# Kernel tuning notes

Measured on AMD Instinct MI355X. Metric: run time of the kernel, lower is better.

## Reference

```python
import jax, jax.numpy as jnp
import numpy as np

N_NODES = 100000
N_EDGES = 1600000
D = 64


def setup_inputs() -> dict:
    key = jax.random.key(0)
    ks = jax.random.split(key, 9)
    x = jax.random.normal(ks[0], (N_NODES, D), dtype=jnp.float32)
    edge_index = jax.random.randint(ks[1], (2, N_EDGES), 0, N_NODES, dtype=jnp.int64)
    edge_attr = jax.random.uniform(ks[2], (N_EDGES,), dtype=jnp.float32)

    def glorot(k, din, dout):
        s = np.sqrt(6.0 / (din + dout)).astype(np.float32)
        return jax.random.uniform(k, (din, dout), jnp.float32, -s, s)

    return {
        "x": x,
        "edge_index": edge_index,
        "edge_attr": edge_attr,
        "W1": glorot(ks[3], D, D), "b1": jnp.zeros((D,), jnp.float32),
        "W2": glorot(ks[4], D, D), "b2": jnp.zeros((D,), jnp.float32),
        "W3": glorot(ks[5], D, D), "b3": jnp.zeros((D,), jnp.float32),
    }


def _gcn_norm(edge_index, edge_weight, n):
    # PyG gcn_norm: add self-loops (weight 1), symmetric D^-1/2 A D^-1/2 normalization.
    src = jnp.concatenate([edge_index[0], jnp.arange(n, dtype=edge_index.dtype)])
    dst = jnp.concatenate([edge_index[1], jnp.arange(n, dtype=edge_index.dtype)])
    w = jnp.concatenate([edge_weight, jnp.ones((n,), edge_weight.dtype)])
    deg = jax.ops.segment_sum(w, dst, num_segments=n)  # in-degree with self-loops
    dinv = jnp.where(deg > 0, jax.lax.rsqrt(deg), 0.0)
    norm = dinv[src] * w * dinv[dst]  # [E+N]
    return src, dst, norm


def _gcn_conv(x, W, b, src, dst, norm, n):
    h = x @ W                                   # linear transform first (PyG GCNConv)
    msg = h[src] * norm[:, None]                # gather + per-edge scale
    out = jax.ops.segment_sum(msg, dst, num_segments=n)  # scatter-add aggregate
    return out + b


def reference(x, edge_index, edge_attr, W1, b1, W2, b2, W3, b3):
    n = x.shape[0]
    src, dst, norm = _gcn_norm(edge_index, edge_attr, n)
    h = jax.nn.relu(_gcn_conv(x, W1, b1, src, dst, norm, n))
    h = jax.nn.relu(_gcn_conv(h, W2, b2, src, dst, norm, n))
    return _gcn_conv(h, W3, b3, src, dst, norm, n)
```

## Files before the change

kernel.cpp:

```cpp
#include <hip/hip_runtime.h>

#define NN 100000
#define NE 1600000
#define DIM 64
#define NPB 128
#define NBIN 782
#define NBINP 1024
#define ECHUNK 2048
#define NCHUNKP 1024

__device__ inline ushort f2bf(float f) {
    unsigned u = __float_as_uint(f);
    unsigned r = u + 0x7FFFu + ((u >> 16) & 1u);
    return (ushort)(r >> 16);
}
__device__ inline float bf2f(ushort h) {
    return __uint_as_float(((unsigned)h) << 16);
}
__device__ inline float bfu(unsigned long long v, int k) {
    return __uint_as_float((unsigned)((v >> (k * 16)) & 0xFFFFu) << 16);
}

__global__ __launch_bounds__(256) void k_hist(const int* __restrict__ dst,
                                              int* __restrict__ gcounts) {
    __shared__ int hist[NBINP];
    int tid = threadIdx.x, chunk = blockIdx.x;
    for (int j = tid; j < NBINP; j += 256) hist[j] = 0;
    __syncthreads();
    int base = chunk * ECHUNK;
    int lim = min(base + ECHUNK, NE);
    for (int i = base + tid; i < lim; i += 256)
        atomicAdd(&hist[dst[i] >> 7], 1);
    __syncthreads();
    for (int j = tid; j < NBINP; j += 256)
        gcounts[j * NCHUNKP + chunk] = hist[j];
}

__global__ __launch_bounds__(256) void k_colscan(int* __restrict__ gcounts,
                                                 int* __restrict__ bintot) {
    __shared__ int sd[256];
    int t = threadIdx.x;
    int* p = gcounts + blockIdx.x * NCHUNKP;
    int v[4], s = 0;
    #pragma unroll
    for (int i = 0; i < 4; i++) { v[i] = p[t * 4 + i]; s += v[i]; }
    sd[t] = s;
    __syncthreads();
    for (int off = 1; off < 256; off <<= 1) {
        int x = (t >= off) ? sd[t - off] : 0;
        __syncthreads();
        sd[t] += x;
        __syncthreads();
    }
    int excl = sd[t] - s;
    #pragma unroll
    for (int i = 0; i < 4; i++) { p[t * 4 + i] = excl; excl += v[i]; }
    if (t == 255) bintot[blockIdx.x] = sd[255];
}

__global__ __launch_bounds__(256) void k_binscan(const int* __restrict__ bintot,
                                                 int* __restrict__ binbase,
                                                 int* __restrict__ row_ptr) {
    __shared__ int sd[256];
    int t = threadIdx.x;
    int v[4], s = 0;
    #pragma unroll
    for (int i = 0; i < 4; i++) { v[i] = bintot[t * 4 + i]; s += v[i]; }
    sd[t] = s;
    __syncthreads();
    for (int off = 1; off < 256; off <<= 1) {
        int x = (t >= off) ? sd[t - off] : 0;
        __syncthreads();
        sd[t] += x;
        __syncthreads();
    }
    int excl = sd[t] - s;
    #pragma unroll
    for (int i = 0; i < 4; i++) { binbase[t * 4 + i] = excl; excl += v[i]; }
    if (t == 255) { binbase[NBINP] = sd[255]; row_ptr[NN] = sd[255]; }
}

__global__ __launch_bounds__(256) void k_scatbin(const int* __restrict__ src,
                                                 const int* __restrict__ dst,
                                                 const float* __restrict__ w,
                                                 const int* __restrict__ gcounts,
                                                 const int* __restrict__ binbase,
                                                 int2* __restrict__ binned) {
    __shared__ int lcur[NBINP];
    int tid = threadIdx.x, chunk = blockIdx.x;
    for (int j = tid; j < NBINP; j += 256) lcur[j] = 0;
    __syncthreads();
    int base = chunk * ECHUNK;
    int lim = min(base + ECHUNK, NE);
    for (int i = base + tid; i < lim; i += 256) {
        int d = dst[i];
        int b = d >> 7;
        int r = atomicAdd(&lcur[b], 1);
        int pos = binbase[b] + gcounts[b * NCHUNKP + chunk] + r;
        int meta = src[i] | ((d & 127) << 17);
        binned[pos] = make_int2(meta, __float_as_int(w[i]));
    }
}

__global__ __launch_bounds__(256) void k_group(const int2* __restrict__ binned,
                                               const int* __restrict__ binbase,
                                               int2* __restrict__ edata,
                                               int* __restrict__ row_ptr,
                                               float* __restrict__ dinv) {
    __shared__ int ndeg[NPB];
    __shared__ float nws[NPB];
    __shared__ int ncur[NPB];
    __shared__ int sd[NPB];
    int t = threadIdx.x, bin = blockIdx.x;
    int beg = binbase[bin], end = binbase[bin + 1];
    if (t < NPB) { ndeg[t] = 0; nws[t] = 0.f; }
    __syncthreads();
    for (int e = beg + t; e < end; e += 256) {
        int2 v = binned[e];
        int dl = ((unsigned)v.x) >> 17;
        atomicAdd(&ndeg[dl], 1);
        atomicAdd(&nws[dl], __int_as_float(v.y));
    }
    __syncthreads();
    int own = 0;
    if (t < NPB) { own = ndeg[t]; sd[t] = own; }
    __syncthreads();
    for (int off = 1; off < NPB; off <<= 1) {
        int x = (t >= off && t < NPB) ? sd[t - off] : 0;
        __syncthreads();
        if (t < NPB) sd[t] += x;
        __syncthreads();
    }
    if (t < NPB) {
        int excl = sd[t] - own;
        ncur[t] = excl;
        int node = bin * NPB + t;
        if (node < NN) {
            row_ptr[node] = beg + excl;
            dinv[node] = rsqrtf(1.0f + nws[t]);
        }
    }
    __syncthreads();
    for (int e = beg + t; e < end; e += 256) {
        int2 v = binned[e];
        int dl = ((unsigned)v.x) >> 17;
        int r = atomicAdd(&ncur[dl], 1);
        edata[beg + r] = make_int2(v.x & 0x1FFFF, v.y);
    }
}

__global__ __launch_bounds__(256) void k_cvt(const float* __restrict__ in,
                                             const float* __restrict__ dinv,
                                             ushort* __restrict__ outb, int total4) {
    int i = blockIdx.x * 256 + threadIdx.x;
    if (i < total4) {
        float dn = dinv[i >> 4];
        float4 v = reinterpret_cast<const float4*>(in)[i];
        ushort4 o;
        o.x = f2bf(v.x * dn); o.y = f2bf(v.y * dn);
        o.z = f2bf(v.z * dn); o.w = f2bf(v.w * dn);
        reinterpret_cast<ushort4*>(outb)[i] = o;
    }
}

#define FMA4U(acc, nm, q) \
    acc.x = fmaf(nm, bfu(q, 0), acc.x); acc.y = fmaf(nm, bfu(q, 1), acc.y); \
    acc.z = fmaf(nm, bfu(q, 2), acc.z); acc.w = fmaf(nm, bfu(q, 3), acc.w);

#define LDROW(idx) (*reinterpret_cast<const unsigned long long*>( \
    Hb + ((size_t)(idx) << 6) + (l << 2)))

template <int RELU>
__global__ __launch_bounds__(256, 8) void k_layer(const int* __restrict__ row_ptr,
                                                  const int2* __restrict__ edata,
                                                  const ushort* __restrict__ Hb,
                                                  const float* __restrict__ W,
                                                  const float* __restrict__ bias,
                                                  const float* __restrict__ dinv,
                                                  ushort* __restrict__ OutB,
                                                  float* __restrict__ OutF, int n) {
    __shared__ float Wlds[64][64];
    __shared__ float rowbuf[4][4][64];
    int tid = threadIdx.x;
    #pragma unroll
    for (int t = tid; t < 4096; t += 256) Wlds[t >> 6][t & 63] = W[t];
    __syncthreads();

    int lane = tid & 63, wv = tid >> 6;
    int g = lane >> 4, l = lane & 15;
    float bl = bias[lane];

    int wave_id = blockIdx.x * 4 + wv;
    int nwaves = gridDim.x * 4;

    for (int base = wave_id * 4; base < n; base += nwaves * 4) {
        int node = base + g;
        bool valid = node < n;
        int beg = 0, end = 0;
        float dn = 0.f;
        if (valid) { beg = row_ptr[node]; end = row_ptr[node + 1]; dn = dinv[node]; }
        unsigned long long svq = LDROW(valid ? node : 0);

        float4 acc = make_float4(0.f, 0.f, 0.f, 0.f);
        int e = beg;
        for (; e + 7 < end; e += 8) {
            int2 ev[8];
            unsigned long long q[8];
            #pragma unroll
            for (int u = 0; u < 8; u++) ev[u] = edata[e + u];
            #pragma unroll
            for (int u = 0; u < 8; u++) q[u] = LDROW(ev[u].x);
            #pragma unroll
            for (int u = 0; u < 8; u++) {
                float nm = __int_as_float(ev[u].y);
                FMA4U(acc, nm, q[u]);
            }
        }
        if (e + 3 < end) {
            int2 ev[4];
            unsigned long long q[4];
            #pragma unroll
            for (int u = 0; u < 4; u++) ev[u] = edata[e + u];
            #pragma unroll
            for (int u = 0; u < 4; u++) q[u] = LDROW(ev[u].x);
            #pragma unroll
            for (int u = 0; u < 4; u++) {
                float nm = __int_as_float(ev[u].y);
                FMA4U(acc, nm, q[u]);
            }
            e += 4;
        }
        if (e + 1 < end) {
            int2 e0 = edata[e], e1 = edata[e + 1];
            unsigned long long q0 = LDROW(e0.x), q1 = LDROW(e1.x);
            float n0 = __int_as_float(e0.y), n1 = __int_as_float(e1.y);
            FMA4U(acc, n0, q0); FMA4U(acc, n1, q1);
            e += 2;
        }
        if (e < end) {
            int2 e0 = edata[e];
            unsigned long long q0 = LDROW(e0.x);
            float n0 = __int_as_float(e0.y);
            FMA4U(acc, n0, q0);
        }

        acc.x = (acc.x + bfu(svq, 0)) * dn;
        acc.y = (acc.y + bfu(svq, 1)) * dn;
        acc.z = (acc.z + bfu(svq, 2)) * dn;
        acc.w = (acc.w + bfu(svq, 3)) * dn;
        *reinterpret_cast<float4*>(&rowbuf[wv][g][l * 4]) = acc;
        __builtin_amdgcn_wave_barrier();

        #pragma unroll 1
        for (int j = 0; j < 4; j++) {
            int onode = base + j;
            if (onode >= n) break;
            float o = 0.f;
            #pragma unroll
            for (int k = 0; k < 64; k++)
                o = fmaf(rowbuf[wv][j][k], Wlds[k][lane], o);
            o += bl;
            if (RELU) {
                o = fmaxf(o, 0.f);
                OutB[(size_t)onode * DIM + lane] = f2bf(o * dinv[onode]);
            } else {
                OutF[(size_t)onode * DIM + lane] = o;
            }
        }
        __builtin_amdgcn_wave_barrier();
    }
}

extern "C" void kernel_launch(void* const* d_in, const int* in_sizes, int n_in,
                              void* d_out, int out_size, void* d_ws, size_t ws_size,
                              hipStream_t stream) {
    const float* x  = (const float*)d_in[0];
    const int* ei   = (const int*)d_in[1];
    const float* ew = (const float*)d_in[2];
    const float* W1 = (const float*)d_in[3];
    const float* b1 = (const float*)d_in[4];
    const float* W2 = (const float*)d_in[5];
    const float* b2 = (const float*)d_in[6];
    const float* W3 = (const float*)d_in[7];
    const float* b3 = (const float*)d_in[8];
    float* out = (float*)d_out;

    const int* src = ei;
    const int* dst = ei + NE;

    auto align = [](size_t v) { return (v + 255) / 256 * 256; };
    char* ws = (char*)d_ws;
    int*   row_ptr = (int*)ws;   ws += align(((size_t)NN + 1) * 4);
    float* dinv    = (float*)ws; ws += align((size_t)NN * 4);
    int2*  edata   = (int2*)ws;  ws += align((size_t)NE * 8);
    char* temp = ws;
    int*  gcounts = (int*)temp;
    int*  bintot  = (int*)(temp + align((size_t)NBINP * NCHUNKP * 4));
    int*  binbase = (int*)((char*)bintot + align((size_t)NBINP * 4));
    int2* binned  = (int2*)((char*)binbase + align(((size_t)NBINP + 1) * 4));
    ws += align((size_t)NBINP * NCHUNKP * 4) + align((size_t)NBINP * 4)
        + align(((size_t)NBINP + 1) * 4) + align((size_t)NE * 8);
    ushort* Hb0 = (ushort*)temp;
    ushort* A1b = (ushort*)ws; ws += align((size_t)NN * DIM * 2);
    ushort* A2b = (ushort*)ws;

    const int gC = (NN * DIM / 4 + 255) / 256;
    const int gL = 2048;

    k_hist<<<NCHUNKP, 256, 0, stream>>>(dst, gcounts);
    k_colscan<<<NBINP, 256, 0, stream>>>(gcounts, bintot);
    k_binscan<<<1, 256, 0, stream>>>(bintot, binbase, row_ptr);
    k_scatbin<<<NCHUNKP, 256, 0, stream>>>(src, dst, ew, gcounts, binbase, binned);
    k_group<<<NBIN, 256, 0, stream>>>(binned, binbase, edata, row_ptr, dinv);
    k_cvt<<<gC, 256, 0, stream>>>(x, dinv, Hb0, NN * DIM / 4);

    k_layer<1><<<gL, 256, 0, stream>>>(row_ptr, edata, Hb0, W1, b1, dinv, A1b, nullptr, NN);
    k_layer<1><<<gL, 256, 0, stream>>>(row_ptr, edata, A1b, W2, b2, dinv, A2b, nullptr, NN);
    k_layer<0><<<gL, 256, 0, stream>>>(row_ptr, edata, A2b, W3, b3, dinv, nullptr, out, NN);
}
```

Measured before the change: 243.2 us.

## Pack edge records into 32 bits with 15-bit weights; fuse x conversion into grouping

```diff
diff --git a/kernel.cpp b/kernel.cpp
--- a/kernel.cpp
+++ b/kernel.cpp
@@ -13,9 +13,6 @@
     unsigned u = __float_as_uint(f);
     unsigned r = u + 0x7FFFu + ((u >> 16) & 1u);
     return (ushort)(r >> 16);
-}
-__device__ inline float bf2f(ushort h) {
-    return __uint_as_float(((unsigned)h) << 16);
 }
 __device__ inline float bfu(unsigned long long v, int k) {
     return __uint_as_float((unsigned)((v >> (k * 16)) & 0xFFFFu) << 16);
@@ -104,9 +101,11 @@
 
 __global__ __launch_bounds__(256) void k_group(const int2* __restrict__ binned,
                                                const int* __restrict__ binbase,
-                                               int2* __restrict__ edata,
+                                               const float* __restrict__ x,
+                                               unsigned* __restrict__ edata,
                                                int* __restrict__ row_ptr,
-                                               float* __restrict__ dinv) {
+                                               float* __restrict__ dinv,
+                                               ushort* __restrict__ Hb0) {
     __shared__ int ndeg[NPB];
     __shared__ float nws[NPB];
     __shared__ int ncur[NPB];
@@ -126,18 +125,20 @@
     if (t < NPB) { own = ndeg[t]; sd[t] = own; }
     __syncthreads();
     for (int off = 1; off < NPB; off <<= 1) {
-        int x = (t >= off && t < NPB) ? sd[t - off] : 0;
-        __syncthreads();
-        if (t < NPB) sd[t] += x;
+        int xx = (t >= off && t < NPB) ? sd[t - off] : 0;
+        __syncthreads();
+        if (t < NPB) sd[t] += xx;
         __syncthreads();
     }
     if (t < NPB) {
         int excl = sd[t] - own;
         ncur[t] = excl;
+        float dv = rsqrtf(1.0f + nws[t]);
+        nws[t] = dv;
         int node = bin * NPB + t;
         if (node < NN) {
             row_ptr[node] = beg + excl;
-            dinv[node] = rsqrtf(1.0f + nws[t]);
+            dinv[node] = dv;
         }
     }
     __syncthreads();
@@ -145,21 +146,19 @@
         int2 v = binned[e];
         int dl = ((unsigned)v.x) >> 17;
         int r = atomicAdd(&ncur[dl], 1);
-        edata[beg + r] = make_int2(v.x & 0x1FFFF, v.y);
-    }
-}
-
-__global__ __launch_bounds__(256) void k_cvt(const float* __restrict__ in,
-                                             const float* __restrict__ dinv,
-                                             ushort* __restrict__ outb, int total4) {
-    int i = blockIdx.x * 256 + threadIdx.x;
-    if (i < total4) {
-        float dn = dinv[i >> 4];
-        float4 v = reinterpret_cast<const float4*>(in)[i];
+        unsigned q15 = __float2uint_rn(__int_as_float(v.y) * 32767.0f);
+        edata[beg + r] = ((unsigned)(v.x & 0x1FFFF) << 15) | q15;
+    }
+    int rowlim = min(NPB, NN - bin * NPB);
+    for (int idx = t; idx < rowlim * 16; idx += 256) {
+        int row = idx >> 4;
+        int node = bin * NPB + row;
+        float dn = nws[row];
+        float4 v = reinterpret_cast<const float4*>(x)[(size_t)node * 16 + (idx & 15)];
         ushort4 o;
         o.x = f2bf(v.x * dn); o.y = f2bf(v.y * dn);
         o.z = f2bf(v.z * dn); o.w = f2bf(v.w * dn);
-        reinterpret_cast<ushort4*>(outb)[i] = o;
+        reinterpret_cast<ushort4*>(Hb0)[(size_t)node * 16 + (idx & 15)] = o;
     }
 }
 
@@ -169,10 +168,11 @@
 
 #define LDROW(idx) (*reinterpret_cast<const unsigned long long*>( \
     Hb + ((size_t)(idx) << 6) + (l << 2)))
+#define DEQ(v) ((float)((v) & 0x7FFFu) * (1.0f / 32767.0f))
 
 template <int RELU>
 __global__ __launch_bounds__(256, 8) void k_layer(const int* __restrict__ row_ptr,
-                                                  const int2* __restrict__ edata,
+                                                  const unsigned* __restrict__ edata,
                                                   const ushort* __restrict__ Hb,
                                                   const float* __restrict__ W,
                                                   const float* __restrict__ bias,
@@ -204,44 +204,42 @@
         float4 acc = make_float4(0.f, 0.f, 0.f, 0.f);
         int e = beg;
         for (; e + 7 < end; e += 8) {
-            int2 ev[8];
+            unsigned ev[8];
             unsigned long long q[8];
             #pragma unroll
             for (int u = 0; u < 8; u++) ev[u] = edata[e + u];
             #pragma unroll
-            for (int u = 0; u < 8; u++) q[u] = LDROW(ev[u].x);
+            for (int u = 0; u < 8; u++) q[u] = LDROW(ev[u] >> 15);
             #pragma unroll
             for (int u = 0; u < 8; u++) {
-                float nm = __int_as_float(ev[u].y);
+                float nm = DEQ(ev[u]);
                 FMA4U(acc, nm, q[u]);
             }
         }
         if (e + 3 < end) {
-            int2 ev[4];
+            unsigned ev[4];
             unsigned long long q[4];
             #pragma unroll
             for (int u = 0; u < 4; u++) ev[u] = edata[e + u];
             #pragma unroll
-            for (int u = 0; u < 4; u++) q[u] = LDROW(ev[u].x);
+            for (int u = 0; u < 4; u++) q[u] = LDROW(ev[u] >> 15);
             #pragma unroll
             for (int u = 0; u < 4; u++) {
-                float nm = __int_as_float(ev[u].y);
+                float nm = DEQ(ev[u]);
                 FMA4U(acc, nm, q[u]);
             }
             e += 4;
         }
         if (e + 1 < end) {
-            int2 e0 = edata[e], e1 = edata[e + 1];
-            unsigned long long q0 = LDROW(e0.x), q1 = LDROW(e1.x);
-            float n0 = __int_as_float(e0.y), n1 = __int_as_float(e1.y);
-            FMA4U(acc, n0, q0); FMA4U(acc, n1, q1);
+            unsigned e0 = edata[e], e1 = edata[e + 1];
+            unsigned long long q0 = LDROW(e0 >> 15), q1 = LDROW(e1 >> 15);
+            FMA4U(acc, DEQ(e0), q0); FMA4U(acc, DEQ(e1), q1);
             e += 2;
         }
         if (e < end) {
-            int2 e0 = edata[e];
-            unsigned long long q0 = LDROW(e0.x);
-            float n0 = __int_as_float(e0.y);
-            FMA4U(acc, n0, q0);
+            unsigned e0 = edata[e];
+            unsigned long long q0 = LDROW(e0 >> 15);
+            FMA4U(acc, DEQ(e0), q0);
         }
 
         acc.x = (acc.x + bfu(svq, 0)) * dn;
@@ -290,29 +288,24 @@
 
     auto align = [](size_t v) { return (v + 255) / 256 * 256; };
     char* ws = (char*)d_ws;
-    int*   row_ptr = (int*)ws;   ws += align(((size_t)NN + 1) * 4);
-    float* dinv    = (float*)ws; ws += align((size_t)NN * 4);
-    int2*  edata   = (int2*)ws;  ws += align((size_t)NE * 8);
-    char* temp = ws;
-    int*  gcounts = (int*)temp;
-    int*  bintot  = (int*)(temp + align((size_t)NBINP * NCHUNKP * 4));
-    int*  binbase = (int*)((char*)bintot + align((size_t)NBINP * 4));
-    int2* binned  = (int2*)((char*)binbase + align(((size_t)NBINP + 1) * 4));
-    ws += align((size_t)NBINP * NCHUNKP * 4) + align((size_t)NBINP * 4)
-        + align(((size_t)NBINP + 1) * 4) + align((size_t)NE * 8);
-    ushort* Hb0 = (ushort*)temp;
-    ushort* A1b = (ushort*)ws; ws += align((size_t)NN * DIM * 2);
-    ushort* A2b = (ushort*)ws;
-
-    const int gC = (NN * DIM / 4 + 255) / 256;
+    int*      row_ptr = (int*)ws;      ws += align(((size_t)NN + 1) * 4);
+    float*    dinv    = (float*)ws;    ws += align((size_t)NN * 4);
+    unsigned* edata   = (unsigned*)ws; ws += align((size_t)NE * 4);
+    ushort*   Hb0     = (ushort*)ws;   ws += align((size_t)NN * DIM * 2);
+    ushort*   A1b     = (ushort*)ws;   ws += align((size_t)NN * DIM * 2);
+    ushort*   A2b     = (ushort*)ws;   ws += align((size_t)NN * DIM * 2);
+    int*  gcounts = (int*)ws;  ws += align((size_t)NBINP * NCHUNKP * 4);
+    int*  bintot  = (int*)ws;  ws += align((size_t)NBINP * 4);
+    int*  binbase = (int*)ws;  ws += align(((size_t)NBINP + 1) * 4);
+    int2* binned  = (int2*)ws;
+
     const int gL = 2048;
 
     k_hist<<<NCHUNKP, 256, 0, stream>>>(dst, gcounts);
     k_colscan<<<NBINP, 256, 0, stream>>>(gcounts, bintot);
     k_binscan<<<1, 256, 0, stream>>>(bintot, binbase, row_ptr);
     k_scatbin<<<NCHUNKP, 256, 0, stream>>>(src, dst, ew, gcounts, binbase, binned);
-    k_group<<<NBIN, 256, 0, stream>>>(binned, binbase, edata, row_ptr, dinv);
-    k_cvt<<<gC, 256, 0, stream>>>(x, dinv, Hb0, NN * DIM / 4);
+    k_group<<<NBIN, 256, 0, stream>>>(binned, binbase, x, edata, row_ptr, dinv, Hb0);
 
     k_layer<1><<<gL, 256, 0, stream>>>(row_ptr, edata, Hb0, W1, b1, dinv, A1b, nullptr, NN);
     k_layer<1><<<gL, 256, 0, stream>>>(row_ptr, edata, A1b, W2, b2, dinv, A2b, nullptr, NN);
```

Measured after the change: 233.7 us. 3.9% less time.
